# Performance work log

Measured on AMD Instinct MI355X. Metric: run time of the kernel, lower is better.

Reference implementation:

```python
import jax, jax.numpy as jnp
import numpy as np

N, E, IN, H = 100000, 400000, 128, 128
HEADS, HC = 4, 128  # GATConv(heads=4, out_channels=128, concat=False)
EPS = 1e-5


def setup_inputs() -> dict:
    key = jax.random.key(0)
    ks = jax.random.split(key, 16)
    rn = lambda i, shape, s=0.05: jax.random.normal(ks[i], shape, jnp.float32) * s
    return {
        "x": jax.random.normal(ks[0], (N, IN), jnp.float32),
        "edge_index": jax.random.randint(ks[1], (2, E), 0, N),
        # SAGEConv1: lin_l (aggregated neighbors, with bias) + lin_r (root)
        "Wl1": rn(2, (IN, H)), "Wr1": rn(3, (IN, H)), "b1": jnp.zeros((H,)),
        "g1": jnp.ones((H,)), "be1": jnp.zeros((H,)),
        # GATConv: shared lin, per-head attention vectors, bias (concat=False -> [HC])
        "Wg": rn(4, (H, HEADS * HC)), "att_s": rn(5, (HEADS, HC)), "att_d": rn(6, (HEADS, HC)), "bg": jnp.zeros((HC,)),
        "g2": jnp.ones((H,)), "be2": jnp.zeros((H,)),
        # SAGEConv3: hidden -> hidden//2
        "Wl3": rn(7, (H, H // 2)), "Wr3": rn(8, (H, H // 2)), "b3": jnp.zeros((H // 2,)),
        "g3": jnp.ones((H // 2,)), "be3": jnp.zeros((H // 2,)),
        # skip: in -> hidden//2
        "Wsk": rn(9, (IN, H // 2)), "bsk": jnp.zeros((H // 2,)),
        # classifier head: 64 -> 64 (BN+ReLU) -> 32 (ReLU) -> 2
        "Wc1": rn(10, (H // 2, 64)), "bc1": jnp.zeros((64,)),
        "gc": jnp.ones((64,)), "bec": jnp.zeros((64,)),
        "Wc2": rn(11, (64, 32)), "bc2": jnp.zeros((32,)),
        "Wc3": rn(12, (32, 2)), "bc3": jnp.zeros((2,)),
    }


def _bn(x, g, b):
    m = x.mean(0)
    v = x.var(0)
    return g * (x - m) * jax.lax.rsqrt(v + EPS) + b


def _sage(x, src, dst, Wl, Wr, b):
    # mean aggregation of neighbor features at dst, then lin_l(agg) + lin_r(x)
    agg = jax.ops.segment_sum(x[src], dst, num_segments=N)
    deg = jax.ops.segment_sum(jnp.ones((src.shape[0],), x.dtype), dst, num_segments=N)
    mean = agg / jnp.maximum(deg, 1.0)[:, None]
    return mean @ Wl + x @ Wr + b


def _gat(x, src, dst, Wg, att_s, att_d, bg):
    xh = (x @ Wg).reshape(N, HEADS, HC)          # [N,H,C]
    a_s = (xh * att_s).sum(-1)                    # [N,H]
    a_d = (xh * att_d).sum(-1)                    # [N,H]
    e = jax.nn.leaky_relu(a_s[src] + a_d[dst], 0.2)   # [E,H]
    emax = jax.lax.stop_gradient(jax.ops.segment_max(e, dst, num_segments=N))
    ee = jnp.exp(e - emax[dst])
    denom = jax.ops.segment_sum(ee, dst, num_segments=N)
    alpha = ee / jnp.maximum(denom, 1e-16)[dst]   # segment softmax over in-edges
    out = jax.ops.segment_sum(alpha[:, :, None] * xh[src], dst, num_segments=N)  # [N,H,C]
    return out.mean(1) + bg                       # concat=False -> mean over heads


def reference(x, edge_index, Wl1, Wr1, b1, g1, be1, Wg, att_s, att_d, bg, g2, be2,
              Wl3, Wr3, b3, g3, be3, Wsk, bsk, Wc1, bc1, gc, bec, Wc2, bc2, Wc3, bc3):
    src, dst = edge_index[0], edge_index[1]
    identity = x @ Wsk + bsk
    h = jax.nn.relu(_bn(_sage(x, src, dst, Wl1, Wr1, b1), g1, be1))
    h = jax.nn.relu(_bn(_gat(h, src, dst, Wg, att_s, att_d, bg), g2, be2))
    h = jax.nn.relu(_bn(_sage(h, src, dst, Wl3, Wr3, b3), g3, be3))
    emb = h + identity
    z = jax.nn.relu(_bn(emb @ Wc1 + bc1, gc, bec))
    z = jax.nn.relu(z @ Wc2 + bc2)
    return jax.nn.log_softmax(z @ Wc3 + bc3, axis=1)
```

## Files before the change

### kernel.cpp

```cpp
#include <hip/hip_runtime.h>
#include <hip/hip_bf16.h>
#include <cmath>


typedef short s16x8 __attribute__((ext_vector_type(8)));
typedef float f32x4 __attribute__((ext_vector_type(4)));

__device__ __forceinline__ float bf2f(unsigned short u) {
  return __uint_as_float((unsigned)u << 16);
}
__device__ __forceinline__ unsigned short f2bf(float f) {
  __hip_bfloat16 h = __float2bfloat16(f);
  return *reinterpret_cast<unsigned short*>(&h);
}

__global__ __launch_bounds__(256) void k_scan1(const int* __restrict__ cnt,
                                               int* __restrict__ bsum, int N) {
  int base = blockIdx.x << 10;
  int t = threadIdx.x;
  int s = 0;
  #pragma unroll
  for (int j = 0; j < 4; ++j) {
    int i = base + t * 4 + j;
    if (i < N) s += cnt[i];
  }
  __shared__ int red[256];
  red[t] = s;
  __syncthreads();
  for (int off = 128; off; off >>= 1) {
    if (t < off) red[t] += red[t + off];
    __syncthreads();
  }
  if (t == 0) bsum[blockIdx.x] = red[0];
}

__global__ __launch_bounds__(1024) void k_scan2(int* __restrict__ bsum, int nb) {
  __shared__ int sh[1024];
  int t = threadIdx.x;
  int v = (t < nb) ? bsum[t] : 0;
  sh[t] = v;
  __syncthreads();
  for (int off = 1; off < 1024; off <<= 1) {
    int u = (t >= off) ? sh[t - off] : 0;
    __syncthreads();
    sh[t] += u;
    __syncthreads();
  }
  if (t < nb) bsum[t] = sh[t] - v;
}

__global__ __launch_bounds__(256) void k_scan3(const int* __restrict__ cnt,
                                               const int* __restrict__ bsum,
                                               int* __restrict__ indptr,
                                               int* __restrict__ cursor, int N) {
  int base = blockIdx.x << 10;
  int t = threadIdx.x;
  int lane = t & 63, w = t >> 6;
  int i0 = base + t * 4;
  int v[4], s = 0;
  #pragma unroll
  for (int j = 0; j < 4; ++j) {
    int i = i0 + j;
    v[j] = (i < N) ? cnt[i] : 0;
    s += v[j];
  }
  int incl = s;
  #pragma unroll
  for (int off = 1; off < 64; off <<= 1) {
    int u = __shfl_up(incl, off);
    if (lane >= off) incl += u;
  }
  __shared__ int wsum[4];
  if (lane == 63) wsum[w] = incl;
  __syncthreads();
  int add = 0;
  for (int j = 0; j < w; ++j) add += wsum[j];
  int run = incl - s + add + bsum[blockIdx.x];
  #pragma unroll
  for (int j = 0; j < 4; ++j) {
    int i = i0 + j;
    if (i < N) {
      cursor[i] = run;
      run += v[j];
      indptr[i + 1] = run;
    }
  }
  if (blockIdx.x == 0 && t == 0) indptr[0] = 0;
}

__global__ void k_fill(const int* __restrict__ src, const int* __restrict__ dst,
                       int* __restrict__ cursor, int* __restrict__ csr_src, int E) {
  int e = blockIdx.x * blockDim.x + threadIdx.x;
  if (e >= E) return;
  int pos = atomicAdd(&cursor[dst[e]], 1);
  csr_src[pos] = src[e];
}

__global__ __launch_bounds__(256) void k_pre(
    const float* __restrict__ x, unsigned short* __restrict__ xbf, long n4,
    const int* __restrict__ dst, int* __restrict__ cnt, int E,
    int gC, int gE,
    const float* __restrict__ Wsk, const float* __restrict__ Wl1,
    const float* __restrict__ Wr1, const float* __restrict__ Wg,
    const float* __restrict__ Wl3, const float* __restrict__ Wr3,
    const float* __restrict__ Wc1, const float* __restrict__ Wc2,
    unsigned short* __restrict__ wt,
    const float* __restrict__ atts, const float* __restrict__ attd,
    float* __restrict__ attw) {
  int bx = blockIdx.x;
  if (bx < gC) {
    long t = (long)bx * 256 + threadIdx.x;
    if (t < n4) {
      float4 v = *reinterpret_cast<const float4*>(x + t * 4);
      ushort4 u;
      u.x = f2bf(v.x); u.y = f2bf(v.y); u.z = f2bf(v.z); u.w = f2bf(v.w);
      *reinterpret_cast<ushort4*>(xbf + t * 4) = u;
    }
    return;
  }
  bx -= gC;
  if (bx < gE) {
    int e = bx * 256 + threadIdx.x;
    if (e < E) atomicAdd(&cnt[dst[e]], 1);
    return;
  }
  bx -= gE;
  if (bx < 504) {
    int t = bx * 256 + threadIdx.x;
    if (t >= 129024) return;
    float v;
    if (t < 8192) {
      int c = t >> 7, k = t & 127;
      v = Wsk[k * 64 + c];
    } else if (t < 24576) {
      int r = t - 8192; int c = r >> 7, k = r & 127;
      v = Wl1[k * 128 + c];
    } else if (t < 40960) {
      int r = t - 24576; int c = r >> 7, k = r & 127;
      v = Wr1[k * 128 + c];
    } else if (t < 106496) {
      int r = t - 40960; int c = r >> 9; int q = r & 511; int h = q >> 7, k = q & 127;
      v = Wg[k * 512 + h * 128 + c];
    } else if (t < 114688) {
      int r = t - 106496; int c = r >> 7, k = r & 127;
      v = Wl3[k * 64 + c];
    } else if (t < 122880) {
      int r = t - 114688; int c = r >> 7, k = r & 127;
      v = Wr3[k * 64 + c];
    } else if (t < 126976) {
      int r = t - 122880; int c = r >> 6, k = r & 63;
      v = Wc1[k * 64 + c];
    } else {
      int r = t - 126976; int c = r >> 6, k = r & 63;
      v = Wc2[k * 32 + c];
    }
    wt[t] = f2bf(v);
    return;
  }
  bx -= 504;
  {
    int t = bx * 256 + threadIdx.x;
    if (t >= 1024) return;
    int k = t >> 3, j = t & 7, h = j & 3;
    const float* av = (j < 4 ? atts : attd) + h * 128;
    const float* wg = Wg + (size_t)k * 512 + h * 128;
    float s = 0.f;
    for (int c = 0; c < 128; ++c) s = fmaf(wg[c], av[c], s);
    attw[t] = s;
  }
}

__device__ __forceinline__ void gmean128_body(const unsigned short* __restrict__ X,
                                              const int* __restrict__ indptr,
                                              const int* __restrict__ csr,
                                              unsigned short* __restrict__ out,
                                              long wid, int lane) {
  int b = indptr[wid], en = indptr[wid + 1];
  float ax = 0.f, ay = 0.f;
  int i = b;
  for (; i + 3 < en; i += 4) {
    int s0 = csr[i], s1 = csr[i + 1], s2 = csr[i + 2], s3 = csr[i + 3];
    ushort2 u0 = *reinterpret_cast<const ushort2*>(X + ((size_t)s0 << 7) + (lane << 1));
    ushort2 u1 = *reinterpret_cast<const ushort2*>(X + ((size_t)s1 << 7) + (lane << 1));
    ushort2 u2 = *reinterpret_cast<const ushort2*>(X + ((size_t)s2 << 7) + (lane << 1));
    ushort2 u3 = *reinterpret_cast<const ushort2*>(X + ((size_t)s3 << 7) + (lane << 1));
    ax += bf2f(u0.x); ay += bf2f(u0.y);
    ax += bf2f(u1.x); ay += bf2f(u1.y);
    ax += bf2f(u2.x); ay += bf2f(u2.y);
    ax += bf2f(u3.x); ay += bf2f(u3.y);
  }
  for (; i < en; ++i) {
    int s = csr[i];
    ushort2 u = *reinterpret_cast<const ushort2*>(X + ((size_t)s << 7) + (lane << 1));
    ax += bf2f(u.x); ay += bf2f(u.y);
  }
  float inv = 1.0f / (float)max(en - b, 1);
  ax *= inv; ay *= inv;
  ushort2 o; o.x = f2bf(ax); o.y = f2bf(ay);
  *reinterpret_cast<ushort2*>(out + (wid << 7) + (lane << 1)) = o;
}

__global__ __launch_bounds__(256) void k_gmean64(const unsigned short* __restrict__ X,
                                                 const int* __restrict__ indptr,
                                                 const int* __restrict__ csr,
                                                 float* __restrict__ out, int N) {
  long wid = ((long)blockIdx.x * blockDim.x + threadIdx.x) >> 6;
  if (wid >= N) return;
  int lane = threadIdx.x & 63;
  int b = indptr[wid], en = indptr[wid + 1];
  float a = 0.f;
  int i = b;
  for (; i + 3 < en; i += 4) {
    int s0 = csr[i], s1 = csr[i + 1], s2 = csr[i + 2], s3 = csr[i + 3];
    unsigned short u0 = X[((size_t)s0 << 6) + lane];
    unsigned short u1 = X[((size_t)s1 << 6) + lane];
    unsigned short u2 = X[((size_t)s2 << 6) + lane];
    unsigned short u3 = X[((size_t)s3 << 6) + lane];
    a += bf2f(u0); a += bf2f(u1); a += bf2f(u2); a += bf2f(u3);
  }
  for (; i < en; ++i) {
    int s = csr[i];
    a += bf2f(X[((size_t)s << 6) + lane]);
  }
  out[(wid << 6) + lane] = a / (float)max(en - b, 1);
}

__global__ __launch_bounds__(256) void k_alpha(const int* __restrict__ indptr,
                                               const int* __restrict__ csr,
                                               const float* __restrict__ asad,
                                               float* __restrict__ alpha, int N) {
  long g = ((long)blockIdx.x * blockDim.x + threadIdx.x) >> 3;
  if (g >= N) return;
  int l8 = threadIdx.x & 7;
  int b = indptr[g], en = indptr[g + 1];
  float4 adv = *reinterpret_cast<const float4*>(asad + g * 8 + 4);
  float m[4] = {-INFINITY, -INFINITY, -INFINITY, -INFINITY};
  for (int i = b + l8; i < en; i += 8) {
    int s = csr[i];
    float4 a = *reinterpret_cast<const float4*>(asad + (size_t)s * 8);
    float e0 = a.x + adv.x, e1 = a.y + adv.y, e2 = a.z + adv.z, e3 = a.w + adv.w;
    e0 = e0 >= 0.f ? e0 : 0.2f * e0; e1 = e1 >= 0.f ? e1 : 0.2f * e1;
    e2 = e2 >= 0.f ? e2 : 0.2f * e2; e3 = e3 >= 0.f ? e3 : 0.2f * e3;
    m[0] = fmaxf(m[0], e0); m[1] = fmaxf(m[1], e1);
    m[2] = fmaxf(m[2], e2); m[3] = fmaxf(m[3], e3);
  }
  #pragma unroll
  for (int off = 1; off < 8; off <<= 1) {
    #pragma unroll
    for (int h = 0; h < 4; ++h) m[h] = fmaxf(m[h], __shfl_xor(m[h], off));
  }
  float den[4] = {0.f, 0.f, 0.f, 0.f};
  for (int i = b + l8; i < en; i += 8) {
    int s = csr[i];
    float4 a = *reinterpret_cast<const float4*>(asad + (size_t)s * 8);
    float e0 = a.x + adv.x, e1 = a.y + adv.y, e2 = a.z + adv.z, e3 = a.w + adv.w;
    e0 = e0 >= 0.f ? e0 : 0.2f * e0; e1 = e1 >= 0.f ? e1 : 0.2f * e1;
    e2 = e2 >= 0.f ? e2 : 0.2f * e2; e3 = e3 >= 0.f ? e3 : 0.2f * e3;
    float4 w;
    w.x = __expf(e0 - m[0]); w.y = __expf(e1 - m[1]);
    w.z = __expf(e2 - m[2]); w.w = __expf(e3 - m[3]);
    den[0] += w.x; den[1] += w.y; den[2] += w.z; den[3] += w.w;
    *reinterpret_cast<float4*>(alpha + (size_t)i * 4) = w;
  }
  #pragma unroll
  for (int off = 1; off < 8; off <<= 1) {
    #pragma unroll
    for (int h = 0; h < 4; ++h) den[h] += __shfl_xor(den[h], off);
  }
  float s0 = 0.25f / fmaxf(den[0], 1e-16f);
  float s1 = 0.25f / fmaxf(den[1], 1e-16f);
  float s2 = 0.25f / fmaxf(den[2], 1e-16f);
  float s3 = 0.25f / fmaxf(den[3], 1e-16f);
  for (int i = b + l8; i < en; i += 8) {
    float4 w = *reinterpret_cast<const float4*>(alpha + (size_t)i * 4);
    w.x *= s0; w.y *= s1; w.z *= s2; w.w *= s3;
    *reinterpret_cast<float4*>(alpha + (size_t)i * 4) = w;
  }
}

__global__ __launch_bounds__(256) void k_gath1(
    const unsigned short* __restrict__ h1, const int* __restrict__ indptr,
    const int* __restrict__ csr, const float* __restrict__ alpha,
    unsigned short* __restrict__ agg, int N) {
  long wid = ((long)blockIdx.x * blockDim.x + threadIdx.x) >> 6;
  if (wid >= N) return;
  int lane = threadIdx.x & 63;
  int b = indptr[wid], en = indptr[wid + 1];
  float a0x = 0.f, a0y = 0.f, a1x = 0.f, a1y = 0.f;
  float a2x = 0.f, a2y = 0.f, a3x = 0.f, a3y = 0.f;
  int i = b;
  for (; i + 3 < en; i += 4) {
    int s0 = csr[i], s1 = csr[i + 1], s2 = csr[i + 2], s3 = csr[i + 3];
    float4 A0 = *reinterpret_cast<const float4*>(alpha + (size_t)i * 4);
    float4 A1 = *reinterpret_cast<const float4*>(alpha + (size_t)(i + 1) * 4);
    float4 A2 = *reinterpret_cast<const float4*>(alpha + (size_t)(i + 2) * 4);
    float4 A3 = *reinterpret_cast<const float4*>(alpha + (size_t)(i + 3) * 4);
    ushort2 u0 = *reinterpret_cast<const ushort2*>(h1 + ((size_t)s0 << 7) + (lane << 1));
    ushort2 u1 = *reinterpret_cast<const ushort2*>(h1 + ((size_t)s1 << 7) + (lane << 1));
    ushort2 u2 = *reinterpret_cast<const ushort2*>(h1 + ((size_t)s2 << 7) + (lane << 1));
    ushort2 u3 = *reinterpret_cast<const ushort2*>(h1 + ((size_t)s3 << 7) + (lane << 1));
    float vx, vy;
    vx = bf2f(u0.x); vy = bf2f(u0.y);
    a0x = fmaf(A0.x, vx, a0x); a0y = fmaf(A0.x, vy, a0y);
    a1x = fmaf(A0.y, vx, a1x); a1y = fmaf(A0.y, vy, a1y);
    a2x = fmaf(A0.z, vx, a2x); a2y = fmaf(A0.z, vy, a2y);
    a3x = fmaf(A0.w, vx, a3x); a3y = fmaf(A0.w, vy, a3y);
    vx = bf2f(u1.x); vy = bf2f(u1.y);
    a0x = fmaf(A1.x, vx, a0x); a0y = fmaf(A1.x, vy, a0y);
    a1x = fmaf(A1.y, vx, a1x); a1y = fmaf(A1.y, vy, a1y);
    a2x = fmaf(A1.z, vx, a2x); a2y = fmaf(A1.z, vy, a2y);
    a3x = fmaf(A1.w, vx, a3x); a3y = fmaf(A1.w, vy, a3y);
    vx = bf2f(u2.x); vy = bf2f(u2.y);
    a0x = fmaf(A2.x, vx, a0x); a0y = fmaf(A2.x, vy, a0y);
    a1x = fmaf(A2.y, vx, a1x); a1y = fmaf(A2.y, vy, a1y);
    a2x = fmaf(A2.z, vx, a2x); a2y = fmaf(A2.z, vy, a2y);
    a3x = fmaf(A2.w, vx, a3x); a3y = fmaf(A2.w, vy, a3y);
    vx = bf2f(u3.x); vy = bf2f(u3.y);
    a0x = fmaf(A3.x, vx, a0x); a0y = fmaf(A3.x, vy, a0y);
    a1x = fmaf(A3.y, vx, a1x); a1y = fmaf(A3.y, vy, a1y);
    a2x = fmaf(A3.z, vx, a2x); a2y = fmaf(A3.z, vy, a2y);
    a3x = fmaf(A3.w, vx, a3x); a3y = fmaf(A3.w, vy, a3y);
  }
  for (; i < en; ++i) {
    int s = csr[i];
    float4 a = *reinterpret_cast<const float4*>(alpha + (size_t)i * 4);
    ushort2 u = *reinterpret_cast<const ushort2*>(h1 + ((size_t)s << 7) + (lane << 1));
    float vx = bf2f(u.x), vy = bf2f(u.y);
    a0x = fmaf(a.x, vx, a0x); a0y = fmaf(a.x, vy, a0y);
    a1x = fmaf(a.y, vx, a1x); a1y = fmaf(a.y, vy, a1y);
    a2x = fmaf(a.z, vx, a2x); a2y = fmaf(a.z, vy, a2y);
    a3x = fmaf(a.w, vx, a3x); a3y = fmaf(a.w, vy, a3y);
  }
  unsigned short* po = agg + ((size_t)wid << 9) + (lane << 1);
  ushort2 o;
  o.x = f2bf(a0x); o.y = f2bf(a0y); *reinterpret_cast<ushort2*>(po)       = o;
  o.x = f2bf(a1x); o.y = f2bf(a1y); *reinterpret_cast<ushort2*>(po + 128) = o;
  o.x = f2bf(a2x); o.y = f2bf(a2y); *reinterpret_cast<ushort2*>(po + 256) = o;
  o.x = f2bf(a3x); o.y = f2bf(a3y); *reinterpret_cast<ushort2*>(po + 384) = o;
}

template <int BNM>
__device__ __forceinline__ ushort4 load_a4(const void* A, int abf, int ldA,
                                           int gr, int col0,
                                           const float* sBN,
                                           const unsigned short* bnadd, int ldAdd) {
  if (BNM == 0) {
    if (abf) {
      return *reinterpret_cast<const ushort4*>(
          (const unsigned short*)A + (size_t)gr * ldA + col0);
    }
    float4 f = *reinterpret_cast<const float4*>(
        (const float*)A + (size_t)gr * ldA + col0);
    ushort4 u;
    u.x = f2bf(f.x); u.y = f2bf(f.y); u.z = f2bf(f.z); u.w = f2bf(f.w);
    return u;
  }
  float v[4];
  if (abf) {
    ushort4 u = *reinterpret_cast<const ushort4*>(
        (const unsigned short*)A + (size_t)gr * ldA + col0);
    v[0] = bf2f(u.x); v[1] = bf2f(u.y); v[2] = bf2f(u.z); v[3] = bf2f(u.w);
  } else {
    float4 f = *reinterpret_cast<const float4*>(
        (const float*)A + (size_t)gr * ldA + col0);
    v[0] = f.x; v[1] = f.y; v[2] = f.z; v[3] = f.w;
  }
  #pragma unroll
  for (int q = 0; q < 4; ++q) {
    int c = col0 + q;
    v[q] = fmaxf(fmaf(sBN[c], v[q], sBN[128 + c]), 0.f);
    if (BNM == 2) v[q] += bf2f(bnadd[(size_t)gr * ldAdd + c]);
  }
  ushort4 u;
  u.x = f2bf(v[0]); u.y = f2bf(v[1]); u.z = f2bf(v[2]); u.w = f2bf(v[3]);
  return u;
}

template <int CF, int BNM>
__device__ __forceinline__ void gemm_body(
    unsigned short* __restrict__ sA, unsigned short* __restrict__ sBt,
    int rowblk,
    const void* __restrict__ A1, int a1bf, int ldA1, int K1,
    const unsigned short* __restrict__ Wt1,
    const void* __restrict__ A2, int a2bf, int ldA2, int K2,
    const unsigned short* __restrict__ Wt2,
    const float* __restrict__ bias, const float* __restrict__ Cadd,
    void* __restrict__ Cout, int obf16,
    int Nrows, int ldC, int relu, float* __restrict__ spart,
    const float* __restrict__ bnst, const float* __restrict__ bng,
    const float* __restrict__ bnbt,
    const unsigned short* __restrict__ bnadd, int ldAdd) {
  constexpr int BN = CF * 32;
  const int tid = threadIdx.x;
  const int lane = tid & 63;
  const int w = tid >> 6;
  const int wr = (w >> 1) * 32;
  const int wc = (w & 1) * (CF * 16);
  const int lr = lane & 15;
  const int lk = (lane >> 4) << 3;
  const int row0 = rowblk * 128;
  const float invN = 1.0f / (float)Nrows;

  const float* bnp = nullptr;
  if constexpr (BNM > 0) {
    __shared__ float sBN[256];
    if (tid < 128 && tid < K1) {
      float m = bnst[tid] * invN;
      float var = bnst[128 + tid] * invN - m * m;
      float sc = bng[tid] * rsqrtf(var + 1e-5f);
      sBN[tid] = sc;
      sBN[128 + tid] = bnbt[tid] - sc * m;
    }
    __syncthreads();
    bnp = sBN;
  }

  f32x4 acc[2][CF];
  #pragma unroll
  for (int i = 0; i < 2; ++i)
    #pragma unroll
    for (int j = 0; j < CF; ++j) acc[i][j] = (f32x4){0.f, 0.f, 0.f, 0.f};

  const int kc = (tid << 2) & 63;
  const int r0 = (tid << 2) >> 6;
  ushort4 aR[4], bR[CF];

  for (int pass = 0; pass < 2; ++pass) {
    const void* A = pass ? A2 : A1;
    if (!A) break;
    const int abf = pass ? a2bf : a1bf;
    const int ldA = pass ? ldA2 : ldA1;
    const int K = pass ? K2 : K1;
    const unsigned short* Wt = pass ? Wt2 : Wt1;

    #pragma unroll
    for (int ii = 0; ii < 4; ++ii) {
      int gr = row0 + r0 + 32 * ii;
      aR[ii] = (gr < Nrows)
                   ? (pass ? load_a4<0>(A, abf, ldA, gr, kc, nullptr, nullptr, 0)
                           : load_a4<BNM>(A, abf, ldA, gr, kc, bnp, bnadd, ldAdd))
                   : make_ushort4(0, 0, 0, 0);
    }
    #pragma unroll
    for (int jj = 0; jj < CF; ++jj)
      bR[jj] = *reinterpret_cast<const ushort4*>(
          Wt + (size_t)(r0 + 32 * jj) * K + kc);

    for (int kb = 0; kb < K; kb += 64) {
      #pragma unroll
      for (int ii = 0; ii < 4; ++ii)
        *reinterpret_cast<ushort4*>(&sA[(r0 + 32 * ii) * 72 + kc]) = aR[ii];
      #pragma unroll
      for (int jj = 0; jj < CF; ++jj)
        *reinterpret_cast<ushort4*>(&sBt[(r0 + 32 * jj) * 72 + kc]) = bR[jj];
      __syncthreads();

      int kn = kb + 64;
      if (kn < K) {
        #pragma unroll
        for (int ii = 0; ii < 4; ++ii) {
          int gr = row0 + r0 + 32 * ii;
          aR[ii] = (gr < Nrows)
                       ? (pass ? load_a4<0>(A, abf, ldA, gr, kn + kc, nullptr, nullptr, 0)
                               : load_a4<BNM>(A, abf, ldA, gr, kn + kc, bnp, bnadd, ldAdd))
                       : make_ushort4(0, 0, 0, 0);
        }
        #pragma unroll
        for (int jj = 0; jj < CF; ++jj)
          bR[jj] = *reinterpret_cast<const ushort4*>(
              Wt + (size_t)(r0 + 32 * jj) * K + kn + kc);
      }

      #pragma unroll
      for (int ki = 0; ki < 2; ++ki) {
        int k0 = lk + ki * 32;
        s16x8 a0 = *reinterpret_cast<const s16x8*>(&sA[(wr + lr) * 72 + k0]);
        s16x8 a1 = *reinterpret_cast<const s16x8*>(&sA[(wr + lr + 16) * 72 + k0]);
        #pragma unroll
        for (int j = 0; j < CF; ++j) {
          s16x8 bj = *reinterpret_cast<const s16x8*>(&sBt[(wc + lr + 16 * j) * 72 + k0]);
          acc[0][j] = __builtin_amdgcn_mfma_f32_16x16x32_bf16(a0, bj, acc[0][j], 0, 0, 0);
          acc[1][j] = __builtin_amdgcn_mfma_f32_16x16x32_bf16(a1, bj, acc[1][j], 0, 0, 0);
        }
      }
      __syncthreads();
    }
  }

  const int rbase = (lane >> 4) << 2;
  float ps[CF], ps2[CF];
  #pragma unroll
  for (int j = 0; j < CF; ++j) { ps[j] = 0.f; ps2[j] = 0.f; }
  #pragma unroll
  for (int i = 0; i < 2; ++i) {
    int grow = row0 + wr + 16 * i + rbase;
    #pragma unroll
    for (int j = 0; j < CF; ++j) {
      int col = wc + 16 * j + lr;
      float bv = bias ? bias[col] : 0.f;
      #pragma unroll
      for (int r = 0; r < 4; ++r) {
        if (grow + r >= Nrows) continue;
        float v = acc[i][j][r] + bv;
        if (Cadd) v += Cadd[(size_t)(grow + r) * ldC + col];
        if (relu) v = fmaxf(v, 0.f);
        ps[j] += v;
        ps2[j] = fmaf(v, v, ps2[j]);
        if (obf16)
          ((unsigned short*)Cout)[(size_t)(grow + r) * ldC + col] = f2bf(v);
        else
          ((float*)Cout)[(size_t)(grow + r) * ldC + col] = v;
      }
    }
  }

  if (spart) {
    #pragma unroll
    for (int j = 0; j < CF; ++j) {
      float a = ps[j], b2 = ps2[j];
      a += __shfl_xor(a, 16); b2 += __shfl_xor(b2, 16);
      a += __shfl_xor(a, 32); b2 += __shfl_xor(b2, 32);
      ps[j] = a; ps2[j] = b2;
    }
    float* sred = reinterpret_cast<float*>(sA);
    if (lane < 16) {
      #pragma unroll
      for (int j = 0; j < CF; ++j) {
        sred[(w * CF + j) * 16 + lane] = ps[j];
        sred[1024 + (w * CF + j) * 16 + lane] = ps2[j];
      }
    }
    __syncthreads();
    int c = tid;
    if (c < BN) {
      int j = (c >= CF * 16) ? (c >> 4) - CF : (c >> 4);
      int wpar = (c >= CF * 16) ? 1 : 0;
      int lr2 = c & 15;
      float s = 0.f, s2 = 0.f;
      for (int ww = wpar; ww < 8; ww += 2) {
        s += sred[(ww * CF + j) * 16 + lr2];
        s2 += sred[1024 + (ww * CF + j) * 16 + lr2];
      }
      spart[(size_t)c * 1024 + rowblk] = s;
      spart[131072 + (size_t)c * 1024 + rowblk] = s2;
    }
  }
}

template <int CF, int BNM>
__global__ __launch_bounds__(512, 4) void k_mgemm(
    const void* __restrict__ A1, int a1bf, int ldA1, int K1,
    const unsigned short* __restrict__ Wt1,
    const void* __restrict__ A2, int a2bf, int ldA2, int K2,
    const unsigned short* __restrict__ Wt2,
    const float* __restrict__ bias, const float* __restrict__ Cadd,
    void* __restrict__ Cout, int obf16,
    int Nrows, int ldC, int relu, float* __restrict__ spart,
    const float* __restrict__ bnst, const float* __restrict__ bng,
    const float* __restrict__ bnbt,
    const unsigned short* __restrict__ bnadd, int ldAdd) {
  __shared__ unsigned short smem[128 * 72 + CF * 32 * 72];
  gemm_body<CF, BNM>(smem, smem + 128 * 72, blockIdx.x,
                     A1, a1bf, ldA1, K1, Wt1, A2, a2bf, ldA2, K2, Wt2,
                     bias, Cadd, Cout, obf16, Nrows, ldC, relu, spart,
                     bnst, bng, bnbt, bnadd, ldAdd);
}

__global__ __launch_bounds__(512, 4) void k_sage1(
    const unsigned short* __restrict__ xbf, const unsigned short* __restrict__ WtSk,
    const float* __restrict__ bsk, unsigned short* __restrict__ idbf,
    const int* __restrict__ indptr, const int* __restrict__ csr,
    unsigned short* __restrict__ mean1bf, int N, int gWsk) {
  if ((int)blockIdx.x < gWsk) {
    __shared__ unsigned short smem[128 * 72 + 64 * 72];
    gemm_body<2, 0>(smem, smem + 128 * 72, blockIdx.x,
                    xbf, 1, 128, 128, WtSk, nullptr, 0, 0, 0, nullptr,
                    bsk, nullptr, idbf, 1, N, 64, 0, nullptr,
                    nullptr, nullptr, nullptr, nullptr, 0);
  } else {
    long wid = (long)(blockIdx.x - gWsk) * 8 + (threadIdx.x >> 6);
    if (wid < N) gmean128_body(xbf, indptr, csr, mean1bf, wid, threadIdx.x & 63);
  }
}

__global__ __launch_bounds__(256) void k_statred(const float* __restrict__ part,
                                                 float* __restrict__ st, int nb) {
  int c = blockIdx.x;
  int t = threadIdx.x;
  float s = 0.f, s2 = 0.f;
  for (int b = t; b < nb; b += 256) {
    s += part[(size_t)c * 1024 + b];
    s2 += part[131072 + (size_t)c * 1024 + b];
  }
  __shared__ float r1[256], r2[256];
  r1[t] = s; r2[t] = s2;
  __syncthreads();
  for (int off = 128; off; off >>= 1) {
    if (t < off) { r1[t] += r1[t + off]; r2[t] += r2[t + off]; }
    __syncthreads();
  }
  if (t == 0) { st[c] = r1[0]; st[128 + c] = r2[0]; }
}

__global__ void k_bnatt(unsigned short* __restrict__ X, const float* __restrict__ stats,
                        const float* __restrict__ g, const float* __restrict__ b,
                        const float* __restrict__ attw,
                        float* __restrict__ asad, int Nrows) {
  int lane = threadIdx.x & 63;
  int c0 = 2 * lane, c1 = 2 * lane + 1;
  float invN = 1.0f / (float)Nrows;
  float m0 = stats[c0] * invN;
  float v0 = stats[128 + c0] * invN - m0 * m0;
  float sc0 = g[c0] * rsqrtf(v0 + 1e-5f);
  float t0 = b[c0] - sc0 * m0;
  float m1 = stats[c1] * invN;
  float v1 = stats[128 + c1] * invN - m1 * m1;
  float sc1 = g[c1] * rsqrtf(v1 + 1e-5f);
  float t1 = b[c1] - sc1 * m1;
  float cA[8], cB[8];
  #pragma unroll
  for (int j = 0; j < 8; ++j) {
    cA[j] = attw[c0 * 8 + j];
    cB[j] = attw[c1 * 8 + j];
  }
  long wid = ((long)blockIdx.x * blockDim.x + threadIdx.x) >> 6;
  long nw = ((long)gridDim.x * blockDim.x) >> 6;
  for (long n = wid; n < Nrows; n += nw) {
    unsigned short* p = X + (n << 7) + (lane << 1);
    ushort2 u = *reinterpret_cast<const ushort2*>(p);
    float y0 = fmaxf(fmaf(sc0, bf2f(u.x), t0), 0.f);
    float y1 = fmaxf(fmaf(sc1, bf2f(u.y), t1), 0.f);
    ushort2 o; o.x = f2bf(y0); o.y = f2bf(y1);
    *reinterpret_cast<ushort2*>(p) = o;
    float a[8];
    #pragma unroll
    for (int j = 0; j < 8; ++j) a[j] = y0 * cA[j] + y1 * cB[j];
    float b4[4];
    #pragma unroll
    for (int j = 0; j < 4; ++j) {
      float keepv = (lane & 32) ? a[j + 4] : a[j];
      float sendv = (lane & 32) ? a[j] : a[j + 4];
      b4[j] = keepv + __shfl_xor(sendv, 32);
    }
    float c2[2];
    #pragma unroll
    for (int j = 0; j < 2; ++j) {
      float keepv = (lane & 16) ? b4[j + 2] : b4[j];
      float sendv = (lane & 16) ? b4[j] : b4[j + 2];
      c2[j] = keepv + __shfl_xor(sendv, 16);
    }
    float keepv = (lane & 8) ? c2[1] : c2[0];
    float sendv = (lane & 8) ? c2[0] : c2[1];
    float d = keepv + __shfl_xor(sendv, 8);
    d += __shfl_xor(d, 4);
    d += __shfl_xor(d, 2);
    d += __shfl_xor(d, 1);
    if ((lane & 7) == 0) asad[n * 8 + (lane >> 3)] = d;
  }
}

__global__ void k_final(const float* __restrict__ z2, const float* __restrict__ W,
                        const float* __restrict__ b, float* __restrict__ out, int Nrows) {
  int n = blockIdx.x * blockDim.x + threadIdx.x;
  if (n >= Nrows) return;
  float l0 = b[0], l1 = b[1];
  const float* z = z2 + (size_t)n * 32;
  #pragma unroll
  for (int k = 0; k < 32; ++k) {
    float v = z[k];
    l0 = fmaf(v, W[2 * k], l0);
    l1 = fmaf(v, W[2 * k + 1], l1);
  }
  float m = fmaxf(l0, l1);
  float lse = m + logf(expf(l0 - m) + expf(l1 - m));
  out[2 * n] = l0 - lse;
  out[2 * n + 1] = l1 - lse;
}

extern "C" void kernel_launch(void* const* d_in, const int* in_sizes, int n_in,
                              void* d_out, int out_size, void* d_ws, size_t ws_size,
                              hipStream_t stream) {
  const float* x    = (const float*)d_in[0];
  const int*   ei   = (const int*)  d_in[1];
  const float* Wl1  = (const float*)d_in[2];
  const float* Wr1  = (const float*)d_in[3];
  const float* b1   = (const float*)d_in[4];
  const float* g1   = (const float*)d_in[5];
  const float* be1  = (const float*)d_in[6];
  const float* Wg   = (const float*)d_in[7];
  const float* atts = (const float*)d_in[8];
  const float* attd = (const float*)d_in[9];
  const float* g2   = (const float*)d_in[11];
  const float* be2  = (const float*)d_in[12];
  const float* Wl3  = (const float*)d_in[13];
  const float* Wr3  = (const float*)d_in[14];
  const float* b3   = (const float*)d_in[15];
  const float* g3   = (const float*)d_in[16];
  const float* be3  = (const float*)d_in[17];
  const float* Wsk  = (const float*)d_in[18];
  const float* bsk  = (const float*)d_in[19];
  const float* Wc1  = (const float*)d_in[20];
  const float* bc1  = (const float*)d_in[21];
  const float* gc   = (const float*)d_in[22];
  const float* bec  = (const float*)d_in[23];
  const float* Wc2  = (const float*)d_in[24];
  const float* bc2  = (const float*)d_in[25];
  const float* Wc3  = (const float*)d_in[26];
  const float* bc3  = (const float*)d_in[27];
  (void)n_in; (void)out_size; (void)ws_size;

  const int N = in_sizes[0] / 128;
  const int E = in_sizes[1] / 2;
  const int* src = ei;
  const int* dst = ei + E;

  auto al4 = [](size_t w) { return (w + 3) & ~(size_t)3; };
  float* ws = (float*)d_ws;
  size_t o = 0;
  int* cnt      = (int*)(ws + o); o += al4((size_t)N);
  int* indptr   = (int*)(ws + o); o += al4((size_t)N + 1);
  int* cursor   = (int*)(ws + o); o += al4((size_t)N);
  int* csr_src  = (int*)(ws + o); o += al4((size_t)E);
  int* bsum     = (int*)(ws + o); o += 1024;
  unsigned short* idbf = (unsigned short*)(ws + o); o += al4((size_t)N * 32);
  float* stats  = ws + o; o += 1024;
  float* spart  = ws + o; o += 262144;
  float* attw   = ws + o; o += 1024;
  float* asad   = ws + o; o += al4((size_t)N * 8);
  float* alpha  = ws + o; o += al4((size_t)E * 4);
  unsigned short* wt = (unsigned short*)(ws + o); o += 64512 + 64;
  float* bufA   = ws + o; o += (size_t)N * 128;
  float* hb1    = ws + o; o += (size_t)N * 64;
  float* hB     = ws + o; o += (size_t)N * 128;
  unsigned short* agg = (unsigned short*)(ws + o); o += (size_t)N * 256;

  unsigned short* xbf     = (unsigned short*)bufA;
  unsigned short* mean1bf = (unsigned short*)(bufA + (size_t)N * 64);
  unsigned short* h1bf    = (unsigned short*)hb1;
  unsigned short* h2bf    = (unsigned short*)bufA;
  unsigned short* yl3     = agg;
  float* mean3f           = (float*)agg + (size_t)N * 32;
  float* h3 = hB;
  float* z1 = bufA + (size_t)N * 64;
  float* z2 = hB + (size_t)N * 64;

  unsigned short* WtSk = wt;
  unsigned short* WtL1 = WtSk + 8192;
  unsigned short* WtR1 = WtL1 + 16384;
  unsigned short* WtG2 = WtR1 + 16384;
  unsigned short* WtL3 = WtG2 + 65536;
  unsigned short* WtR3 = WtL3 + 8192;
  unsigned short* WtC1 = WtR3 + 8192;
  unsigned short* WtC2 = WtC1 + 4096;

  float* st1 = stats, *st2 = stats + 256, *st3 = stats + 512, *st4 = stats + 768;

  dim3 blk(256);
  dim3 blk512(512);
  int gE     = (E + 255) / 256;
  int gN128  = (N + 127) / 128;
  int gSC    = (N + 1023) / 1024;
  int gW     = (int)(((long)N * 64 + 255) / 256);
  int gA     = (int)(((long)N * 8 + 255) / 256);
  int gC     = (int)(((long)N * 32 + 255) / 256);
  int gGM8   = (N + 7) / 8;

  hipMemsetAsync(cnt, 0, (size_t)N * 4, stream);

  k_pre<<<gC + gE + 504 + 4, blk, 0, stream>>>(
      x, xbf, (long)N * 32, dst, cnt, E, gC, gE,
      Wsk, Wl1, Wr1, Wg, Wl3, Wr3, Wc1, Wc2, wt, atts, attd, attw);
  k_scan1<<<gSC, blk, 0, stream>>>(cnt, bsum, N);
  k_scan2<<<1, 1024, 0, stream>>>(bsum, gSC);
  k_scan3<<<gSC, blk, 0, stream>>>(cnt, bsum, indptr, cursor, N);
  k_fill<<<gE, blk, 0, stream>>>(src, dst, cursor, csr_src, E);

  k_sage1<<<gN128 + gGM8, blk512, 0, stream>>>(
      xbf, WtSk, bsk, idbf, indptr, csr_src, mean1bf, N, gN128);
  k_mgemm<4, 0><<<dim3(gN128, 1), blk512, 0, stream>>>(
      mean1bf, 1, 128, 128, WtL1, xbf, 1, 128, 128, WtR1,
      b1, nullptr, h1bf, 1, N, 128, 0, spart,
      nullptr, nullptr, nullptr, nullptr, 0);
  k_statred<<<128, blk, 0, stream>>>(spart, st1, gN128);

  k_bnatt<<<2048, blk, 0, stream>>>(h1bf, st1, g1, be1, attw, asad, N);
  k_alpha<<<gA, blk, 0, stream>>>(indptr, csr_src, asad, alpha, N);
  k_gath1<<<gW, blk, 0, stream>>>(h1bf, indptr, csr_src, alpha, agg, N);
  k_mgemm<4, 0><<<dim3(gN128, 1), blk512, 0, stream>>>(
      agg, 1, 512, 512, WtG2, nullptr, 0, 0, 0, nullptr,
      nullptr, nullptr, h2bf, 1, N, 128, 0, spart,
      nullptr, nullptr, nullptr, nullptr, 0);
  k_statred<<<128, blk, 0, stream>>>(spart, st2, gN128);

  k_mgemm<2, 1><<<dim3(gN128, 1), blk512, 0, stream>>>(
      h2bf, 1, 128, 128, WtL3, nullptr, 0, 0, 0, nullptr,
      nullptr, nullptr, yl3, 1, N, 64, 0, nullptr,
      st2, g2, be2, nullptr, 0);
  k_gmean64<<<gW, blk, 0, stream>>>(yl3, indptr, csr_src, mean3f, N);
  k_mgemm<2, 1><<<dim3(gN128, 1), blk512, 0, stream>>>(
      h2bf, 1, 128, 128, WtR3, nullptr, 0, 0, 0, nullptr,
      b3, mean3f, h3, 0, N, 64, 0, spart,
      st2, g2, be2, nullptr, 0);
  k_statred<<<64, blk, 0, stream>>>(spart, st3, gN128);

  k_mgemm<2, 2><<<dim3(gN128, 1), blk512, 0, stream>>>(
      h3, 0, 64, 64, WtC1, nullptr, 0, 0, 0, nullptr,
      bc1, nullptr, z1, 0, N, 64, 0, spart,
      st3, g3, be3, idbf, 64);
  k_statred<<<64, blk, 0, stream>>>(spart, st4, gN128);
  k_mgemm<1, 1><<<dim3(gN128, 1), blk512, 0, stream>>>(
      z1, 0, 64, 64, WtC2, nullptr, 0, 0, 0, nullptr,
      bc2, nullptr, z2, 0, N, 32, 1, nullptr,
      st4, gc, bec, nullptr, 0);
  k_final<<<(N + 255) / 256, blk, 0, stream>>>(z2, Wc3, bc3, (float*)d_out, N);
}
```

Measured before the change: 457.5 us.

## Merge SAGE3 left and right GEMMs into one launch with separate add-stats pass

The two SAGE3 GEMMs (the neighbor projection and the root projection) now run as one kernel whose grid is split in half, so they execute concurrently instead of being serialized around the mean aggregation. The root projection no longer waits on the aggregated mean. A new elementwise kernel adds the aggregated mean into the root output and computes the per-channel BN partial sums. This trades one GEMM launch and its epilogue for an extra read-modify-write pass over the N×64 float tensor.

New measurement: 447.0 us. -2.3%, faster.

```diff
diff --git a/kernel.cpp b/kernel.cpp
--- a/kernel.cpp
+++ b/kernel.cpp
@@ -583,6 +583,51 @@
   }
 }
 
+__global__ __launch_bounds__(512, 4) void k_sage3(
+    const unsigned short* __restrict__ h2bf,
+    const unsigned short* __restrict__ WtL3, const unsigned short* __restrict__ WtR3,
+    unsigned short* __restrict__ yl3, float* __restrict__ h3p,
+    const float* __restrict__ b3,
+    const float* __restrict__ st2, const float* __restrict__ g2,
+    const float* __restrict__ be2, int N, int gHalf) {
+  __shared__ unsigned short smem[128 * 72 + 64 * 72];
+  if ((int)blockIdx.x < gHalf) {
+    gemm_body<2, 1>(smem, smem + 128 * 72, blockIdx.x,
+                    h2bf, 1, 128, 128, WtL3, nullptr, 0, 0, 0, nullptr,
+                    nullptr, nullptr, yl3, 1, N, 64, 0, nullptr,
+                    st2, g2, be2, nullptr, 0);
+  } else {
+    gemm_body<2, 1>(smem, smem + 128 * 72, blockIdx.x - gHalf,
+                    h2bf, 1, 128, 128, WtR3, nullptr, 0, 0, 0, nullptr,
+                    b3, nullptr, h3p, 0, N, 64, 0, nullptr,
+                    st2, g2, be2, nullptr, 0);
+  }
+}
+
+__global__ __launch_bounds__(256) void k_addstats(
+    float* __restrict__ X, const float* __restrict__ add, long n,
+    float* __restrict__ spart) {
+  int c = threadIdx.x & 63;
+  float s = 0.f, s2 = 0.f;
+  for (long i = (long)blockIdx.x * 256 + threadIdx.x; i < n; i += 262144) {
+    float v = X[i] + add[i];
+    X[i] = v;
+    s += v;
+    s2 = fmaf(v, v, s2);
+  }
+  __shared__ float r1[256], r2[256];
+  r1[threadIdx.x] = s; r2[threadIdx.x] = s2;
+  __syncthreads();
+  if (threadIdx.x < 64) {
+    float a = r1[threadIdx.x] + r1[threadIdx.x + 64] + r1[threadIdx.x + 128] +
+              r1[threadIdx.x + 192];
+    float b = r2[threadIdx.x] + r2[threadIdx.x + 64] + r2[threadIdx.x + 128] +
+              r2[threadIdx.x + 192];
+    spart[(size_t)c * 1024 + blockIdx.x] = a;
+    spart[131072 + (size_t)c * 1024 + blockIdx.x] = b;
+  }
+}
+
 __global__ __launch_bounds__(256) void k_statred(const float* __restrict__ part,
                                                  float* __restrict__ st, int nb) {
   int c = blockIdx.x;
@@ -792,16 +837,11 @@
       nullptr, nullptr, nullptr, nullptr, 0);
   k_statred<<<128, blk, 0, stream>>>(spart, st2, gN128);
 
-  k_mgemm<2, 1><<<dim3(gN128, 1), blk512, 0, stream>>>(
-      h2bf, 1, 128, 128, WtL3, nullptr, 0, 0, 0, nullptr,
-      nullptr, nullptr, yl3, 1, N, 64, 0, nullptr,
-      st2, g2, be2, nullptr, 0);
+  k_sage3<<<2 * gN128, blk512, 0, stream>>>(
+      h2bf, WtL3, WtR3, yl3, h3, b3, st2, g2, be2, N, gN128);
   k_gmean64<<<gW, blk, 0, stream>>>(yl3, indptr, csr_src, mean3f, N);
-  k_mgemm<2, 1><<<dim3(gN128, 1), blk512, 0, stream>>>(
-      h2bf, 1, 128, 128, WtR3, nullptr, 0, 0, 0, nullptr,
-      b3, mean3f, h3, 0, N, 64, 0, spart,
-      st2, g2, be2, nullptr, 0);
-  k_statred<<<64, blk, 0, stream>>>(spart, st3, gN128);
+  k_addstats<<<1024, blk, 0, stream>>>(h3, mean3f, (long)N * 64, spart);
+  k_statred<<<64, blk, 0, stream>>>(spart, st3, 1024);
 
   k_mgemm<2, 2><<<dim3(gN128, 1), blk512, 0, stream>>>(
       h3, 0, 64, 64, WtC1, nullptr, 0, 0, 0, nullptr,
```
